# Kernel tuning notes

Hardware: AMD Instinct MI355X
Metric: run time of the kernel (lower is better)

Reference implementation:

```python
import jax, jax.numpy as jnp
import numpy as np

D_MODEL = 512
NHEAD = 8
HEAD_DIM = D_MODEL // NHEAD
DFF = 2048
RANK = 64
L = 1024
N = 8
EPS = 1e-5


def _layer_norm(x, g, b):
    m = jnp.mean(x, axis=-1, keepdims=True)
    v = jnp.mean(jnp.square(x - m), axis=-1, keepdims=True)
    return (x - m) * jax.lax.rsqrt(v + EPS) * g + b


def setup_inputs() -> dict:
    key = jax.random.key(0)
    ks = jax.random.split(key, 20)
    s = 1.0 / np.sqrt(D_MODEL)
    inp = {
        "q": jax.random.normal(ks[0], (L, N, D_MODEL), jnp.float32),
        "k": jax.random.normal(ks[1], (L, N, D_MODEL), jnp.float32),
        "v": jax.random.normal(ks[2], (L, N, D_MODEL), jnp.float32),
        # attention projections, stored (in, out) so x @ W
        "Wq": jax.random.normal(ks[3], (D_MODEL, D_MODEL), jnp.float32) * s,
        "bq": jnp.zeros((D_MODEL,), jnp.float32),
        "Wk": jax.random.normal(ks[4], (D_MODEL, D_MODEL), jnp.float32) * s,
        "bk": jnp.zeros((D_MODEL,), jnp.float32),
        "Wv": jax.random.normal(ks[5], (D_MODEL, D_MODEL), jnp.float32) * s,
        "bv": jnp.zeros((D_MODEL,), jnp.float32),
        "Wo": jax.random.normal(ks[6], (D_MODEL, D_MODEL), jnp.float32) * s,
        "bo": jnp.zeros((D_MODEL,), jnp.float32),
        "topk": jnp.float32(0.3),  # learned scalar, k = int(S * sigmoid(topk))
        "A1": jax.random.normal(ks[7], (D_MODEL, RANK), jnp.float32) * s,
        "B1": jax.random.normal(ks[8], (RANK, DFF), jnp.float32) / np.sqrt(RANK),
        "A2": jax.random.normal(ks[9], (DFF, RANK), jnp.float32) / np.sqrt(DFF),
        "B2": jax.random.normal(ks[10], (RANK, D_MODEL), jnp.float32) / np.sqrt(RANK),
        "g1": jnp.ones((D_MODEL,), jnp.float32),
        "be1": jnp.zeros((D_MODEL,), jnp.float32),
        "g2": jnp.ones((D_MODEL,), jnp.float32),
        "be2": jnp.zeros((D_MODEL,), jnp.float32),
    }
    return inp


def reference(q, k, v, Wq, bq, Wk, bk, Wv, bv, Wo, bo, topk,
              A1, B1, A2, B2, g1, be1, g2, be2):
    Lq, Nb, E = q.shape
    S = k.shape[0]
    H, Dh = NHEAD, HEAD_DIM

    # projections -> (N, L, H, Dh)
    qh = (q @ Wq + bq).reshape(Lq, Nb, H, Dh).transpose(1, 0, 2, 3)
    kh = (k @ Wk + bk).reshape(S, Nb, H, Dh).transpose(1, 0, 2, 3)
    vh = (v @ Wv + bv).reshape(S, Nb, H, Dh).transpose(1, 0, 2, 3)

    scores = jnp.einsum('nlhd,nshd->nlhs', qh, kh) / jnp.sqrt(jnp.float32(Dh))

    # dynamic top-k mask: keep the k = int(S * sigmoid(topk)) largest per row
    k_keep = (S * jax.nn.sigmoid(topk)).astype(jnp.int32)  # 588 for topk=0.3
    sorted_desc = jnp.sort(scores, axis=-1)[..., ::-1]
    idx = jnp.broadcast_to(k_keep - 1, scores.shape[:-1])[..., None]
    thresh = jnp.take_along_axis(sorted_desc, idx, axis=-1)  # k-th largest
    masked = jnp.where(scores >= thresh, scores, -jnp.inf)
    attn_w = jax.nn.softmax(masked, axis=-1)

    # note original flattens (d, h) order: 'nlhs,nshd->nldh' then view(L,N,E)
    ao = jnp.einsum('nlhs,nshd->nldh', attn_w, vh)
    ao = ao.transpose(1, 0, 2, 3).reshape(Lq, Nb, E)
    attn_out = ao @ Wo + bo

    src = _layer_norm(q + attn_out, g1, be1)
    ffn = jax.nn.relu(src @ A1 @ B1) @ A2 @ B2
    src = _layer_norm(src + ffn, g2, be2)
    return src
```

## Files before the change

### kernel.cpp

```cpp
#include <hip/hip_runtime.h>

typedef unsigned short u16;
typedef unsigned int u32;
using s16x8 = __attribute__((ext_vector_type(8))) short;
using s16x4 = __attribute__((ext_vector_type(4))) short;
using u16x4 = __attribute__((ext_vector_type(4))) unsigned short;
using u32x4 = __attribute__((ext_vector_type(4))) unsigned int;
using f32x4 = __attribute__((ext_vector_type(4))) float;

__device__ __forceinline__ u16 f2bf(float f) {
  unsigned int u = __float_as_uint(f);
  u += 0x7FFFu + ((u >> 16) & 1u);
  return (u16)(u >> 16);
}
__device__ __forceinline__ float bf2f(u16 b) {
  return __uint_as_float(((u32)b) << 16);
}
__device__ __forceinline__ u32 pkbf(float a, float b) {
  u32 r;
  asm("v_cvt_pk_bf16_f32 %0, %1, %2" : "=v"(r) : "v"(a), "v"(b));
  return r;
}
__device__ __forceinline__ u32 f2key(float f) {
  u32 u = __float_as_uint(f);
  u32 flip = (u32)((int)u >> 31) | 0x80000000u;
  return (u ^ flip) >> 16;
}
__device__ __forceinline__ float key2f(u32 k) {
  u32 t = k << 16;
  u32 msk = ((int)t < 0) ? 0x80000000u : 0xFFFF0000u;
  return __uint_as_float(t ^ msk);
}

__global__ __launch_bounds__(256) void prep_w(
    const float* __restrict__ Wq, const float* __restrict__ Wk, const float* __restrict__ Wv,
    const float* __restrict__ Wo, const float* __restrict__ A1, const float* __restrict__ B1,
    const float* __restrict__ A2, const float* __restrict__ B2,
    u16* __restrict__ WqT, u16* __restrict__ WkT, u16* __restrict__ WvT, u16* __restrict__ WoT,
    u16* __restrict__ A1T, u16* __restrict__ B1T, u16* __restrict__ A2T, u16* __restrict__ B2T) {
  __shared__ u16 t[64][68];
  int b = blockIdx.x, tid = threadIdx.x;
  const float* src; u16* dst; int base, R, C;
  if (b < 64)        { src = Wq; dst = WqT; base = 0;   R = 512;  C = 512; }
  else if (b < 128)  { src = Wk; dst = WkT; base = 64;  R = 512;  C = 512; }
  else if (b < 192)  { src = Wv; dst = WvT; base = 128; R = 512;  C = 512; }
  else if (b < 256)  { src = Wo; dst = WoT; base = 192; R = 512;  C = 512; }
  else if (b < 264)  { src = A1; dst = A1T; base = 256; R = 512;  C = 64;  }
  else if (b < 296)  { src = B1; dst = B1T; base = 264; R = 64;   C = 2048;}
  else if (b < 328)  { src = A2; dst = A2T; base = 296; R = 2048; C = 64;  }
  else               { src = B2; dst = B2T; base = 328; R = 64;   C = 512; }
  int ti = b - base;
  int tpr = C >> 6;
  int r0 = (ti / tpr) * 64, c0 = (ti % tpr) * 64;
#pragma unroll
  for (int i = 0; i < 4; ++i) {
    int r = i * 16 + (tid >> 4), c = (tid & 15) * 4;
    float4 f = *(const float4*)&src[(size_t)(r0 + r) * C + c0 + c];
    t[r][c] = f2bf(f.x); t[r][c + 1] = f2bf(f.y);
    t[r][c + 2] = f2bf(f.z); t[r][c + 3] = f2bf(f.w);
  }
  __syncthreads();
#pragma unroll
  for (int i = 0; i < 4; ++i) {
    int cc = i * 16 + (tid >> 4), rr = (tid & 15) * 4;
    u16x4 o;
    o[0] = t[rr][cc]; o[1] = t[rr + 1][cc]; o[2] = t[rr + 2][cc]; o[3] = t[rr + 3][cc];
    *(u16x4*)&dst[(size_t)(c0 + cc) * R + r0 + rr] = o;
  }
}

__global__ __launch_bounds__(256, 4) void qkv_fused(
    const float* __restrict__ q, const float* __restrict__ k, const float* __restrict__ v,
    const u16* __restrict__ WqT, const u16* __restrict__ WkT, const u16* __restrict__ WvT,
    const float* __restrict__ bq, const float* __restrict__ bk, const float* __restrict__ bv,
    u16* __restrict__ Qw, u16* __restrict__ Kw, u16* __restrict__ Vw) {
  __shared__ __align__(16) u16 As[128][72];
  __shared__ __align__(16) u16 Bs[128][72];
  const int z = blockIdx.z;
  const float* A = z == 0 ? q : (z == 1 ? k : v);
  const u16* Bt = z == 0 ? WqT : (z == 1 ? WkT : WvT);
  const float* bias = z == 0 ? bq : (z == 1 ? bk : bv);
  u16* outp = z == 0 ? Qw : (z == 1 ? Kw : Vw);

  const int tid = threadIdx.x;
  const int m0 = blockIdx.y * 128, n0 = blockIdx.x * 128;
  const int lane = tid & 63, wid = tid >> 6;
  const int l16 = lane & 15, hi = lane >> 4;
  const int wr = (wid >> 1) * 64, wc = (wid & 1) * 64;

  f32x4 acc[4][4];
#pragma unroll
  for (int i = 0; i < 4; ++i)
#pragma unroll
    for (int j = 0; j < 4; ++j) acc[i][j] = (f32x4){0.f, 0.f, 0.f, 0.f};

  for (int k0 = 0; k0 < 512; k0 += 64) {
    if (k0) __syncthreads();
#pragma unroll
    for (int i = 0; i < 4; ++i) {
      int idx = i * 256 + tid;
      int r = idx >> 3, cc = (idx & 7) * 8;
      float4 f0 = *(const float4*)&A[(size_t)(m0 + r) * 512 + k0 + cc];
      float4 f1 = *(const float4*)&A[(size_t)(m0 + r) * 512 + k0 + cc + 4];
      u32x4 pk;
      pk[0] = pkbf(f0.x, f0.y); pk[1] = pkbf(f0.z, f0.w);
      pk[2] = pkbf(f1.x, f1.y); pk[3] = pkbf(f1.z, f1.w);
      *(u32x4*)&As[r][cc] = pk;
      *(s16x8*)&Bs[r][cc] = *(const s16x8*)&Bt[(size_t)(n0 + r) * 512 + k0 + cc];
    }
    __syncthreads();
#pragma unroll
    for (int kk = 0; kk < 2; ++kk) {
      const int kb_ = kk * 32 + hi * 8;
      s16x8 af[4], bf[4];
#pragma unroll
      for (int mf = 0; mf < 4; ++mf) af[mf] = *(const s16x8*)&As[wr + mf * 16 + l16][kb_];
#pragma unroll
      for (int nf = 0; nf < 4; ++nf) bf[nf] = *(const s16x8*)&Bs[wc + nf * 16 + l16][kb_];
#pragma unroll
      for (int mf = 0; mf < 4; ++mf)
#pragma unroll
        for (int nf = 0; nf < 4; ++nf)
          acc[mf][nf] = __builtin_amdgcn_mfma_f32_16x16x32_bf16(af[mf], bf[nf], acc[mf][nf], 0, 0, 0);
    }
  }

#pragma unroll
  for (int mf = 0; mf < 4; ++mf)
#pragma unroll
    for (int nf = 0; nf < 4; ++nf)
#pragma unroll
      for (int i = 0; i < 4; ++i) {
        int row = m0 + wr + mf * 16 + hi * 4 + i;
        int col = n0 + wc + nf * 16 + l16;
        float val = acc[mf][nf][i] + bias[col];
        if (z == 0) val *= 0.18033688f;
        int l = row >> 3, n = row & 7, hh = col >> 6, d = col & 63;
        if (z < 2)
          outp[(((size_t)(n * 8 + hh) * 1024 + l) << 6) + d] = f2bf(val);
        else
          outp[((size_t)(n * 8 + hh) * 64 + d) * 1024 + l] = f2bf(val);
      }
}

__global__ __launch_bounds__(512, 4) void attn_kernel(const u16* __restrict__ Qw,
                                                      const u16* __restrict__ Kw,
                                                      const u16* __restrict__ Vw,
                                                      const float* __restrict__ topk,
                                                      u16* __restrict__ ao) {
  __shared__ __align__(16) u16 scb[32 * 1024];
  __shared__ __align__(16) u16 Qt[32][72];
  __shared__ float invs[32];
  const int tid = threadIdx.x, lane = tid & 63, wid = tid >> 6;
  const int l16 = lane & 15, hi = lane >> 4;
  const int mb = blockIdx.x, nh = blockIdx.y;

  const int kkeep = (int)(1024.f / (1.f + __expf(-topk[0])));

  {
    int r = tid >> 4, dc = (tid & 15) << 2;
    *(s16x4*)&Qt[r][dc] =
        *(const s16x4*)&Qw[((size_t)nh * 1024 + mb * 32 + r) * 64 + dc];
  }
  __syncthreads();

  {
    const u16* Kb = Kw + (size_t)nh * 1024 * 64;
    s16x8 bq0[2], bq1[2];
#pragma unroll
    for (int qh = 0; qh < 2; ++qh) {
      bq0[qh] = *(const s16x8*)&Qt[qh * 16 + l16][hi * 8];
      bq1[qh] = *(const s16x8*)&Qt[qh * 16 + l16][32 + hi * 8];
    }
    const int s0 = wid * 128;
#pragma unroll
    for (int nf = 0; nf < 8; ++nf) {
      const int sr = s0 + nf * 16 + l16;
      s16x8 a0 = *(const s16x8*)&Kb[(size_t)sr * 64 + hi * 8];
      s16x8 a1 = *(const s16x8*)&Kb[(size_t)sr * 64 + 32 + hi * 8];
#pragma unroll
      for (int qh = 0; qh < 2; ++qh) {
        f32x4 acc = {0.f, 0.f, 0.f, 0.f};
        acc = __builtin_amdgcn_mfma_f32_16x16x32_bf16(a0, bq0[qh], acc, 0, 0, 0);
        acc = __builtin_amdgcn_mfma_f32_16x16x32_bf16(a1, bq1[qh], acc, 0, 0, 0);
        const int row_q = qh * 16 + l16;
        u32 k0 = f2key(acc[0]) | (f2key(acc[1]) << 16);
        u32 k1 = f2key(acc[2]) | (f2key(acc[3]) << 16);
        char* rowq = (char*)scb + row_q * 2048;
        int boff = (2 * (s0 + nf * 16 + 4 * hi)) ^ ((row_q & 7) << 4);
        *(uint2*)(rowq + boff) = make_uint2(k0, k1);
      }
    }
  }
  __syncthreads();

  {
    const int r = wid * 4;
    char* rb0 = (char*)scb + (r + 0) * 2048;
    char* rb1 = (char*)scb + (r + 1) * 2048;
    char* rb2 = (char*)scb + (r + 2) * 2048;
    char* rb3 = (char*)scb + (r + 3) * 2048;
    const int X0 = ((r + 0) & 7) << 4, X1 = ((r + 1) & 7) << 4;
    const int X2 = ((r + 2) & 7) << 4, X3 = ((r + 3) & 7) << 4;
    u32 k0a[16], k1a[16], k2a[16], k3a[16];
#pragma unroll
    for (int c = 0; c < 8; ++c) {
      u32 w0 = *(const u32*)(rb0 + ((4 * lane + 256 * c) ^ X0));
      u32 w1 = *(const u32*)(rb1 + ((4 * lane + 256 * c) ^ X1));
      u32 w2 = *(const u32*)(rb2 + ((4 * lane + 256 * c) ^ X2));
      u32 w3 = *(const u32*)(rb3 + ((4 * lane + 256 * c) ^ X3));
      k0a[2 * c] = w0 & 0xFFFFu; k0a[2 * c + 1] = w0 >> 16;
      k1a[2 * c] = w1 & 0xFFFFu; k1a[2 * c + 1] = w1 >> 16;
      k2a[2 * c] = w2 & 0xFFFFu; k2a[2 * c + 1] = w2 >> 16;
      k3a[2 * c] = w3 & 0xFFFFu; k3a[2 * c + 1] = w3 >> 16;
    }
    u32 T0 = 0, T1 = 0, T2 = 0, T3 = 0;
    for (int bit = 15; bit >= 0; --bit) {
      const u32 bb = 1u << bit;
      u32 c0 = T0 + bb, c1 = T1 + bb, c2 = T2 + bb, c3 = T3 + bb;
      int n0 = 0, n1 = 0, n2 = 0, n3 = 0;
#pragma unroll
      for (int j = 0; j < 16; ++j) {
        n0 += __popcll(__ballot(k0a[j] >= c0));
        n1 += __popcll(__ballot(k1a[j] >= c1));
        n2 += __popcll(__ballot(k2a[j] >= c2));
        n3 += __popcll(__ballot(k3a[j] >= c3));
      }
      T0 = (n0 >= kkeep) ? c0 : T0;
      T1 = (n1 >= kkeep) ? c1 : T1;
      T2 = (n2 >= kkeep) ? c2 : T2;
      T3 = (n3 >= kkeep) ? c3 : T3;
    }
    const float tv0 = key2f(T0), tv1 = key2f(T1), tv2 = key2f(T2), tv3 = key2f(T3);
    float s0 = 0.f, s1 = 0.f, s2 = 0.f, s3 = 0.f;
#pragma unroll
    for (int c = 0; c < 8; ++c) {
      {
        u32 ka = k0a[2 * c], kb = k0a[2 * c + 1];
        float e0 = (ka >= T0) ? __builtin_amdgcn_exp2f(key2f(ka) - tv0) : 0.f;
        float e1 = (kb >= T0) ? __builtin_amdgcn_exp2f(key2f(kb) - tv0) : 0.f;
        s0 += e0 + e1;
        *(u32*)(rb0 + ((4 * lane + 256 * c) ^ X0)) = pkbf(e0, e1);
      }
      {
        u32 ka = k1a[2 * c], kb = k1a[2 * c + 1];
        float e0 = (ka >= T1) ? __builtin_amdgcn_exp2f(key2f(ka) - tv1) : 0.f;
        float e1 = (kb >= T1) ? __builtin_amdgcn_exp2f(key2f(kb) - tv1) : 0.f;
        s1 += e0 + e1;
        *(u32*)(rb1 + ((4 * lane + 256 * c) ^ X1)) = pkbf(e0, e1);
      }
      {
        u32 ka = k2a[2 * c], kb = k2a[2 * c + 1];
        float e0 = (ka >= T2) ? __builtin_amdgcn_exp2f(key2f(ka) - tv2) : 0.f;
        float e1 = (kb >= T2) ? __builtin_amdgcn_exp2f(key2f(kb) - tv2) : 0.f;
        s2 += e0 + e1;
        *(u32*)(rb2 + ((4 * lane + 256 * c) ^ X2)) = pkbf(e0, e1);
      }
      {
        u32 ka = k3a[2 * c], kb = k3a[2 * c + 1];
        float e0 = (ka >= T3) ? __builtin_amdgcn_exp2f(key2f(ka) - tv3) : 0.f;
        float e1 = (kb >= T3) ? __builtin_amdgcn_exp2f(key2f(kb) - tv3) : 0.f;
        s3 += e0 + e1;
        *(u32*)(rb3 + ((4 * lane + 256 * c) ^ X3)) = pkbf(e0, e1);
      }
    }
#pragma unroll
    for (int off = 1; off < 64; off <<= 1) {
      s0 += __shfl_xor(s0, off);
      s1 += __shfl_xor(s1, off);
      s2 += __shfl_xor(s2, off);
      s3 += __shfl_xor(s3, off);
    }
    if (lane == 0) {
      invs[r + 0] = __builtin_amdgcn_rcpf(s0);
      invs[r + 1] = __builtin_amdgcn_rcpf(s1);
      invs[r + 2] = __builtin_amdgcn_rcpf(s2);
      invs[r + 3] = __builtin_amdgcn_rcpf(s3);
    }
  }
  __syncthreads();

  {
    const u16* Vb = Vw + (size_t)nh * 64 * 1024;
    const int rh = wid >> 2, d0 = (wid & 3) * 16;
    f32x4 oacc0 = {0.f, 0.f, 0.f, 0.f};
    f32x4 oacc1 = {0.f, 0.f, 0.f, 0.f};
    const char* Pbase = (const char*)scb + (rh * 16 + l16) * 2048;
    const int Xp = (l16 & 7) << 4;
#pragma unroll
    for (int ks = 0; ks < 32; ks += 2) {
      int kb0 = (ks * 64 + hi * 16) ^ Xp;
      int kb1 = ((ks + 1) * 64 + hi * 16) ^ Xp;
      s16x8 a0 = *(const s16x8*)(Pbase + kb0);
      s16x8 a1 = *(const s16x8*)(Pbase + kb1);
      s16x8 b0 = *(const s16x8*)&Vb[(size_t)(d0 + l16) * 1024 + ks * 32 + hi * 8];
      s16x8 b1 = *(const s16x8*)&Vb[(size_t)(d0 + l16) * 1024 + (ks + 1) * 32 + hi * 8];
      oacc0 = __builtin_amdgcn_mfma_f32_16x16x32_bf16(a0, b0, oacc0, 0, 0, 0);
      oacc1 = __builtin_amdgcn_mfma_f32_16x16x32_bf16(a1, b1, oacc1, 0, 0, 0);
    }
    const int n = nh >> 3, hh = nh & 7;
#pragma unroll
    for (int i = 0; i < 4; ++i) {
      int l = mb * 32 + rh * 16 + hi * 4 + i;
      int d = d0 + l16;
      float vv = (oacc0[i] + oacc1[i]) * invs[rh * 16 + hi * 4 + i];
      ao[(size_t)(l * 8 + n) * 512 + d * 8 + hh] = f2bf(vv);
    }
  }
}

template <bool FIRST>
__global__ __launch_bounds__(256, 2) void gemm_ln(const u16* __restrict__ A,
                                                  const u16* __restrict__ Bt,
                                                  const float* __restrict__ bias,
                                                  const float* __restrict__ residf,
                                                  const u16* __restrict__ residb,
                                                  const float* __restrict__ g,
                                                  const float* __restrict__ be,
                                                  float* __restrict__ outf,
                                                  u16* __restrict__ outb) {
  constexpr int K = FIRST ? 512 : 64;
  __shared__ __align__(16) u16 As[16][72];
  __shared__ float red_s[4][16];
  __shared__ float red_q[4][16];
  const int tid = threadIdx.x;
  const int lane = tid & 63, wid = tid >> 6;
  const int l16 = lane & 15, hi = lane >> 4;
  const int m0 = blockIdx.x * 16;
  const int wc = wid * 128;

  f32x4 acc[8];
#pragma unroll
  for (int nf = 0; nf < 8; ++nf) acc[nf] = (f32x4){0.f, 0.f, 0.f, 0.f};

  for (int k0 = 0; k0 < K; k0 += 64) {
    if (k0) __syncthreads();
    {
      int r = tid >> 4, c = (tid & 15) << 2;
      *(s16x4*)&As[r][c] = *(const s16x4*)&A[(size_t)(m0 + r) * K + k0 + c];
    }
    __syncthreads();
#pragma unroll
    for (int kk = 0; kk < 2; ++kk) {
      const int kb_ = kk * 32 + hi * 8;
      s16x8 a = *(const s16x8*)&As[l16][kb_];
#pragma unroll
      for (int nf = 0; nf < 8; ++nf) {
        s16x8 b = *(const s16x8*)&Bt[(size_t)(wc + nf * 16 + l16) * K + k0 + kb_];
        acc[nf] = __builtin_amdgcn_mfma_f32_16x16x32_bf16(a, b, acc[nf], 0, 0, 0);
      }
    }
  }

#pragma unroll
  for (int nf = 0; nf < 8; ++nf) {
    int col = wc + nf * 16 + l16;
#pragma unroll
    for (int i = 0; i < 4; ++i) {
      float v = acc[nf][i];
      int row = m0 + hi * 4 + i;
      if (FIRST) v += bias[col] + residf[(size_t)row * 512 + col];
      else v += bf2f(residb[(size_t)row * 512 + col]);
      acc[nf][i] = v;
    }
  }
  float s[4] = {0.f, 0.f, 0.f, 0.f}, q2[4] = {0.f, 0.f, 0.f, 0.f};
#pragma unroll
  for (int nf = 0; nf < 8; ++nf)
#pragma unroll
    for (int i = 0; i < 4; ++i) {
      s[i] += acc[nf][i];
      q2[i] += acc[nf][i] * acc[nf][i];
    }
#pragma unroll
  for (int i = 0; i < 4; ++i) {
#pragma unroll
    for (int off = 1; off < 16; off <<= 1) {
      s[i] += __shfl_xor(s[i], off);
      q2[i] += __shfl_xor(q2[i], off);
    }
  }
  if (l16 == 0) {
#pragma unroll
    for (int i = 0; i < 4; ++i) {
      red_s[wid][hi * 4 + i] = s[i];
      red_q[wid][hi * 4 + i] = q2[i];
    }
  }
  __syncthreads();
  float mean[4], rstd[4];
#pragma unroll
  for (int i = 0; i < 4; ++i) {
    int r = hi * 4 + i;
    float ms = red_s[0][r] + red_s[1][r] + red_s[2][r] + red_s[3][r];
    float mq = red_q[0][r] + red_q[1][r] + red_q[2][r] + red_q[3][r];
    mean[i] = ms * (1.f / 512.f);
    float var = mq * (1.f / 512.f) - mean[i] * mean[i];
    rstd[i] = rsqrtf(var + 1e-5f);
  }
#pragma unroll
  for (int nf = 0; nf < 8; ++nf) {
    int col = wc + nf * 16 + l16;
    float gv = g[col], bev = be[col];
#pragma unroll
    for (int i = 0; i < 4; ++i) {
      int row = m0 + hi * 4 + i;
      float y = (acc[nf][i] - mean[i]) * rstd[i] * gv + bev;
      if (FIRST) outb[(size_t)row * 512 + col] = f2bf(y);
      else outf[(size_t)row * 512 + col] = y;
    }
  }
}

__global__ __launch_bounds__(256, 4) void ffn3(const u16* __restrict__ srcb,
                                               const u16* __restrict__ A1T,
                                               const u16* __restrict__ B1T,
                                               const u16* __restrict__ A2T,
                                               u16* __restrict__ w2) {
  __shared__ __align__(16) u16 As[32][72];
  __shared__ __align__(16) u16 Bs[64][72];
  __shared__ __align__(16) u16 Us[32][72];
  __shared__ __align__(16) u16 B1s[64][72];
  __shared__ __align__(16) u16 A2s[64][72];
  __shared__ __align__(16) u16 Hs[32][72];
  const int tid = threadIdx.x;
  const int lane = tid & 63, wid = tid >> 6;
  const int l16 = lane & 15, hi = lane >> 4;
  const int m0 = blockIdx.x * 32;
  const int wm = (wid & 1) * 16, wn = (wid >> 1) * 32;

  f32x4 accu[2];
  accu[0] = (f32x4){0.f, 0.f, 0.f, 0.f};
  accu[1] = (f32x4){0.f, 0.f, 0.f, 0.f};
  for (int k0 = 0; k0 < 512; k0 += 64) {
    if (k0) __syncthreads();
    {
      int r = tid >> 3, c = (tid & 7) << 3;
      *(s16x8*)&As[r][c] = *(const s16x8*)&srcb[(size_t)(m0 + r) * 512 + k0 + c];
    }
#pragma unroll
    for (int i = 0; i < 2; ++i) {
      int idx = i * 256 + tid;
      int r = idx >> 3, c = (idx & 7) << 3;
      *(s16x8*)&Bs[r][c] = *(const s16x8*)&A1T[(size_t)r * 512 + k0 + c];
    }
    __syncthreads();
#pragma unroll
    for (int kk = 0; kk < 2; ++kk) {
      const int kb_ = kk * 32 + hi * 8;
      s16x8 a = *(const s16x8*)&As[wm + l16][kb_];
#pragma unroll
      for (int j = 0; j < 2; ++j) {
        s16x8 b = *(const s16x8*)&Bs[wn + j * 16 + l16][kb_];
        accu[j] = __builtin_amdgcn_mfma_f32_16x16x32_bf16(a, b, accu[j], 0, 0, 0);
      }
    }
  }
  __syncthreads();
#pragma unroll
  for (int j = 0; j < 2; ++j)
#pragma unroll
    for (int i = 0; i < 4; ++i)
      Us[wm + hi * 4 + i][wn + j * 16 + l16] = f2bf(accu[j][i]);

  f32x4 w2a[2];
  w2a[0] = (f32x4){0.f, 0.f, 0.f, 0.f};
  w2a[1] = (f32x4){0.f, 0.f, 0.f, 0.f};
  for (int jc = 0; jc < 32; ++jc) {
#pragma unroll
    for (int i = 0; i < 2; ++i) {
      int idx = i * 256 + tid;
      int r = idx >> 3, c = (idx & 7) << 3;
      *(s16x8*)&B1s[r][c] = *(const s16x8*)&B1T[(size_t)(jc * 64 + r) * 64 + c];
      *(s16x8*)&A2s[r][c] = *(const s16x8*)&A2T[(size_t)r * 2048 + jc * 64 + c];
    }
    __syncthreads();
    f32x4 ha[2];
    ha[0] = (f32x4){0.f, 0.f, 0.f, 0.f};
    ha[1] = (f32x4){0.f, 0.f, 0.f, 0.f};
#pragma unroll
    for (int kk = 0; kk < 2; ++kk) {
      const int kb_ = kk * 32 + hi * 8;
      s16x8 a = *(const s16x8*)&Us[wm + l16][kb_];
#pragma unroll
      for (int j = 0; j < 2; ++j) {
        s16x8 b = *(const s16x8*)&B1s[wn + j * 16 + l16][kb_];
        ha[j] = __builtin_amdgcn_mfma_f32_16x16x32_bf16(a, b, ha[j], 0, 0, 0);
      }
    }
#pragma unroll
    for (int j = 0; j < 2; ++j)
#pragma unroll
      for (int i = 0; i < 4; ++i)
        Hs[wm + hi * 4 + i][wn + j * 16 + l16] = f2bf(fmaxf(ha[j][i], 0.f));
    __syncthreads();
#pragma unroll
    for (int kk = 0; kk < 2; ++kk) {
      const int kb_ = kk * 32 + hi * 8;
      s16x8 a = *(const s16x8*)&Hs[wm + l16][kb_];
#pragma unroll
      for (int j = 0; j < 2; ++j) {
        s16x8 b = *(const s16x8*)&A2s[wn + j * 16 + l16][kb_];
        w2a[j] = __builtin_amdgcn_mfma_f32_16x16x32_bf16(a, b, w2a[j], 0, 0, 0);
      }
    }
    __syncthreads();
  }
#pragma unroll
  for (int j = 0; j < 2; ++j)
#pragma unroll
    for (int i = 0; i < 4; ++i)
      w2[(size_t)(m0 + wm + hi * 4 + i) * 64 + wn + j * 16 + l16] = f2bf(w2a[j][i]);
}

extern "C" void kernel_launch(void* const* d_in, const int* in_sizes, int n_in,
                              void* d_out, int out_size, void* d_ws, size_t ws_size,
                              hipStream_t stream) {
  const float* q = (const float*)d_in[0];
  const float* k = (const float*)d_in[1];
  const float* v = (const float*)d_in[2];
  const float* Wq = (const float*)d_in[3];
  const float* bq = (const float*)d_in[4];
  const float* Wk = (const float*)d_in[5];
  const float* bk = (const float*)d_in[6];
  const float* Wv = (const float*)d_in[7];
  const float* bv = (const float*)d_in[8];
  const float* Wo = (const float*)d_in[9];
  const float* bo = (const float*)d_in[10];
  const float* topk = (const float*)d_in[11];
  const float* A1 = (const float*)d_in[12];
  const float* B1 = (const float*)d_in[13];
  const float* A2 = (const float*)d_in[14];
  const float* B2 = (const float*)d_in[15];
  const float* g1 = (const float*)d_in[16];
  const float* be1 = (const float*)d_in[17];
  const float* g2 = (const float*)d_in[18];
  const float* be2 = (const float*)d_in[19];

  char* ws = (char*)d_ws;
  constexpr size_t SZ_TOK_BF = (size_t)8192 * 512 * 2;
  constexpr size_t SZ_W_BF = (size_t)512 * 512 * 2;
  constexpr size_t O_QW = 0;
  constexpr size_t O_KW = O_QW + SZ_TOK_BF;
  constexpr size_t O_VW = O_KW + SZ_TOK_BF;
  constexpr size_t O_WQT = O_VW + SZ_TOK_BF;
  constexpr size_t O_WKT = O_WQT + SZ_W_BF;
  constexpr size_t O_WVT = O_WKT + SZ_W_BF;
  constexpr size_t O_WOT = O_WVT + SZ_W_BF;
  constexpr size_t O_A1T = O_WOT + SZ_W_BF;
  constexpr size_t O_B1T = O_A1T + 65536;
  constexpr size_t O_A2T = O_B1T + 262144;
  constexpr size_t O_B2T = O_A2T + 262144;
  constexpr size_t O_AO = O_B2T + 65536;
  constexpr size_t O_SRCB = O_AO + SZ_TOK_BF;
  constexpr size_t O_W2 = O_SRCB + SZ_TOK_BF;

  u16* Qw_ = (u16*)(ws + O_QW);
  u16* Kw_ = (u16*)(ws + O_KW);
  u16* Vw_ = (u16*)(ws + O_VW);
  u16* WqT = (u16*)(ws + O_WQT);
  u16* WkT = (u16*)(ws + O_WKT);
  u16* WvT = (u16*)(ws + O_WVT);
  u16* WoT = (u16*)(ws + O_WOT);
  u16* A1T = (u16*)(ws + O_A1T);
  u16* B1T = (u16*)(ws + O_B1T);
  u16* A2T = (u16*)(ws + O_A2T);
  u16* B2T = (u16*)(ws + O_B2T);
  u16* ao = (u16*)(ws + O_AO);
  u16* srcb = (u16*)(ws + O_SRCB);
  u16* w2 = (u16*)(ws + O_W2);

  prep_w<<<336, 256, 0, stream>>>(Wq, Wk, Wv, Wo, A1, B1, A2, B2,
                                  WqT, WkT, WvT, WoT, A1T, B1T, A2T, B2T);

  qkv_fused<<<dim3(4, 64, 3), 256, 0, stream>>>(q, k, v, WqT, WkT, WvT,
                                                bq, bk, bv, Qw_, Kw_, Vw_);

  attn_kernel<<<dim3(32, 64), 512, 0, stream>>>(Qw_, Kw_, Vw_, topk, ao);

  gemm_ln<true><<<512, 256, 0, stream>>>(ao, WoT, bo, q, nullptr, g1, be1, nullptr, srcb);

  ffn3<<<256, 256, 0, stream>>>(srcb, A1T, B1T, A2T, w2);

  gemm_ln<false><<<512, 256, 0, stream>>>(w2, B2T, nullptr, nullptr, srcb, g2, be2,
                                          (float*)d_out, nullptr);
}
```

Before: 286.6 us.

## Pre-convert q/k/v to bf16, prefetch K/V fragments, vectorize score LDS traffic

```diff
diff --git a/kernel.cpp b/kernel.cpp
--- a/kernel.cpp
+++ b/kernel.cpp
@@ -32,14 +32,27 @@
   return __uint_as_float(t ^ msk);
 }
 
-__global__ __launch_bounds__(256) void prep_w(
+__global__ __launch_bounds__(256) void prep_all(
+    const float* __restrict__ q, const float* __restrict__ k, const float* __restrict__ v,
     const float* __restrict__ Wq, const float* __restrict__ Wk, const float* __restrict__ Wv,
     const float* __restrict__ Wo, const float* __restrict__ A1, const float* __restrict__ B1,
     const float* __restrict__ A2, const float* __restrict__ B2,
+    u16* __restrict__ qb, u16* __restrict__ kb, u16* __restrict__ vb,
     u16* __restrict__ WqT, u16* __restrict__ WkT, u16* __restrict__ WvT, u16* __restrict__ WoT,
     u16* __restrict__ A1T, u16* __restrict__ B1T, u16* __restrict__ A2T, u16* __restrict__ B2T) {
   __shared__ u16 t[64][68];
   int b = blockIdx.x, tid = threadIdx.x;
+  if (b < 12288) {
+    const float* src = b < 4096 ? q : (b < 8192 ? k : v);
+    u16* dst = b < 4096 ? qb : (b < 8192 ? kb : vb);
+    int i = (b & 4095) * 256 + tid;
+    float4 f = ((const float4*)src)[i];
+    u16x4 o;
+    o[0] = f2bf(f.x); o[1] = f2bf(f.y); o[2] = f2bf(f.z); o[3] = f2bf(f.w);
+    ((u16x4*)dst)[i] = o;
+    return;
+  }
+  b -= 12288;
   const float* src; u16* dst; int base, R, C;
   if (b < 64)        { src = Wq; dst = WqT; base = 0;   R = 512;  C = 512; }
   else if (b < 128)  { src = Wk; dst = WkT; base = 64;  R = 512;  C = 512; }
@@ -70,14 +83,14 @@
 }
 
 __global__ __launch_bounds__(256, 4) void qkv_fused(
-    const float* __restrict__ q, const float* __restrict__ k, const float* __restrict__ v,
+    const u16* __restrict__ qb, const u16* __restrict__ kb, const u16* __restrict__ vb,
     const u16* __restrict__ WqT, const u16* __restrict__ WkT, const u16* __restrict__ WvT,
     const float* __restrict__ bq, const float* __restrict__ bk, const float* __restrict__ bv,
     u16* __restrict__ Qw, u16* __restrict__ Kw, u16* __restrict__ Vw) {
   __shared__ __align__(16) u16 As[128][72];
   __shared__ __align__(16) u16 Bs[128][72];
   const int z = blockIdx.z;
-  const float* A = z == 0 ? q : (z == 1 ? k : v);
+  const u16* A = z == 0 ? qb : (z == 1 ? kb : vb);
   const u16* Bt = z == 0 ? WqT : (z == 1 ? WkT : WvT);
   const float* bias = z == 0 ? bq : (z == 1 ? bk : bv);
   u16* outp = z == 0 ? Qw : (z == 1 ? Kw : Vw);
@@ -100,12 +113,7 @@
     for (int i = 0; i < 4; ++i) {
       int idx = i * 256 + tid;
       int r = idx >> 3, cc = (idx & 7) * 8;
-      float4 f0 = *(const float4*)&A[(size_t)(m0 + r) * 512 + k0 + cc];
-      float4 f1 = *(const float4*)&A[(size_t)(m0 + r) * 512 + k0 + cc + 4];
-      u32x4 pk;
-      pk[0] = pkbf(f0.x, f0.y); pk[1] = pkbf(f0.z, f0.w);
-      pk[2] = pkbf(f1.x, f1.y); pk[3] = pkbf(f1.z, f1.w);
-      *(u32x4*)&As[r][cc] = pk;
+      *(s16x8*)&As[r][cc] = *(const s16x8*)&A[(size_t)(m0 + r) * 512 + k0 + cc];
       *(s16x8*)&Bs[r][cc] = *(const s16x8*)&Bt[(size_t)(n0 + r) * 512 + k0 + cc];
     }
     __syncthreads();
@@ -173,16 +181,22 @@
       bq1[qh] = *(const s16x8*)&Qt[qh * 16 + l16][32 + hi * 8];
     }
     const int s0 = wid * 128;
+    const size_t kbase = (size_t)(s0 + l16) * 64 + hi * 8;
+    s16x8 c0 = *(const s16x8*)&Kb[kbase];
+    s16x8 c1 = *(const s16x8*)&Kb[kbase + 32];
 #pragma unroll
     for (int nf = 0; nf < 8; ++nf) {
-      const int sr = s0 + nf * 16 + l16;
-      s16x8 a0 = *(const s16x8*)&Kb[(size_t)sr * 64 + hi * 8];
-      s16x8 a1 = *(const s16x8*)&Kb[(size_t)sr * 64 + 32 + hi * 8];
+      s16x8 n0_, n1_;
+      if (nf < 7) {
+        const size_t nb = kbase + (size_t)(nf + 1) * 1024;
+        n0_ = *(const s16x8*)&Kb[nb];
+        n1_ = *(const s16x8*)&Kb[nb + 32];
+      }
 #pragma unroll
       for (int qh = 0; qh < 2; ++qh) {
         f32x4 acc = {0.f, 0.f, 0.f, 0.f};
-        acc = __builtin_amdgcn_mfma_f32_16x16x32_bf16(a0, bq0[qh], acc, 0, 0, 0);
-        acc = __builtin_amdgcn_mfma_f32_16x16x32_bf16(a1, bq1[qh], acc, 0, 0, 0);
+        acc = __builtin_amdgcn_mfma_f32_16x16x32_bf16(c0, bq0[qh], acc, 0, 0, 0);
+        acc = __builtin_amdgcn_mfma_f32_16x16x32_bf16(c1, bq1[qh], acc, 0, 0, 0);
         const int row_q = qh * 16 + l16;
         u32 k0 = f2key(acc[0]) | (f2key(acc[1]) << 16);
         u32 k1 = f2key(acc[2]) | (f2key(acc[3]) << 16);
@@ -190,6 +204,7 @@
         int boff = (2 * (s0 + nf * 16 + 4 * hi)) ^ ((row_q & 7) << 4);
         *(uint2*)(rowq + boff) = make_uint2(k0, k1);
       }
+      c0 = n0_; c1 = n1_;
     }
   }
   __syncthreads();
@@ -202,17 +217,25 @@
     char* rb3 = (char*)scb + (r + 3) * 2048;
     const int X0 = ((r + 0) & 7) << 4, X1 = ((r + 1) & 7) << 4;
     const int X2 = ((r + 2) & 7) << 4, X3 = ((r + 3) & 7) << 4;
+    const int o0 = (16 * lane) ^ X0, o0b = (16 * lane + 1024) ^ X0;
+    const int o1 = (16 * lane) ^ X1, o1b = (16 * lane + 1024) ^ X1;
+    const int o2 = (16 * lane) ^ X2, o2b = (16 * lane + 1024) ^ X2;
+    const int o3 = (16 * lane) ^ X3, o3b = (16 * lane + 1024) ^ X3;
+    u32x4 q0a = *(const u32x4*)(rb0 + o0), q0b = *(const u32x4*)(rb0 + o0b);
+    u32x4 q1a = *(const u32x4*)(rb1 + o1), q1b = *(const u32x4*)(rb1 + o1b);
+    u32x4 q2a = *(const u32x4*)(rb2 + o2), q2b = *(const u32x4*)(rb2 + o2b);
+    u32x4 q3a = *(const u32x4*)(rb3 + o3), q3b = *(const u32x4*)(rb3 + o3b);
     u32 k0a[16], k1a[16], k2a[16], k3a[16];
 #pragma unroll
-    for (int c = 0; c < 8; ++c) {
-      u32 w0 = *(const u32*)(rb0 + ((4 * lane + 256 * c) ^ X0));
-      u32 w1 = *(const u32*)(rb1 + ((4 * lane + 256 * c) ^ X1));
-      u32 w2 = *(const u32*)(rb2 + ((4 * lane + 256 * c) ^ X2));
-      u32 w3 = *(const u32*)(rb3 + ((4 * lane + 256 * c) ^ X3));
-      k0a[2 * c] = w0 & 0xFFFFu; k0a[2 * c + 1] = w0 >> 16;
-      k1a[2 * c] = w1 & 0xFFFFu; k1a[2 * c + 1] = w1 >> 16;
-      k2a[2 * c] = w2 & 0xFFFFu; k2a[2 * c + 1] = w2 >> 16;
-      k3a[2 * c] = w3 & 0xFFFFu; k3a[2 * c + 1] = w3 >> 16;
+    for (int j = 0; j < 4; ++j) {
+      k0a[2 * j] = q0a[j] & 0xFFFFu; k0a[2 * j + 1] = q0a[j] >> 16;
+      k0a[8 + 2 * j] = q0b[j] & 0xFFFFu; k0a[9 + 2 * j] = q0b[j] >> 16;
+      k1a[2 * j] = q1a[j] & 0xFFFFu; k1a[2 * j + 1] = q1a[j] >> 16;
+      k1a[8 + 2 * j] = q1b[j] & 0xFFFFu; k1a[9 + 2 * j] = q1b[j] >> 16;
+      k2a[2 * j] = q2a[j] & 0xFFFFu; k2a[2 * j + 1] = q2a[j] >> 16;
+      k2a[8 + 2 * j] = q2b[j] & 0xFFFFu; k2a[9 + 2 * j] = q2b[j] >> 16;
+      k3a[2 * j] = q3a[j] & 0xFFFFu; k3a[2 * j + 1] = q3a[j] >> 16;
+      k3a[8 + 2 * j] = q3b[j] & 0xFFFFu; k3a[9 + 2 * j] = q3b[j] >> 16;
     }
     u32 T0 = 0, T1 = 0, T2 = 0, T3 = 0;
     for (int bit = 15; bit >= 0; --bit) {
@@ -233,37 +256,46 @@
     }
     const float tv0 = key2f(T0), tv1 = key2f(T1), tv2 = key2f(T2), tv3 = key2f(T3);
     float s0 = 0.f, s1 = 0.f, s2 = 0.f, s3 = 0.f;
-#pragma unroll
-    for (int c = 0; c < 8; ++c) {
+    u32x4 w0a, w0b, w1a, w1b, w2a_, w2b, w3a, w3b;
+#pragma unroll
+    for (int j = 0; j < 4; ++j) {
       {
-        u32 ka = k0a[2 * c], kb = k0a[2 * c + 1];
-        float e0 = (ka >= T0) ? __builtin_amdgcn_exp2f(key2f(ka) - tv0) : 0.f;
-        float e1 = (kb >= T0) ? __builtin_amdgcn_exp2f(key2f(kb) - tv0) : 0.f;
-        s0 += e0 + e1;
-        *(u32*)(rb0 + ((4 * lane + 256 * c) ^ X0)) = pkbf(e0, e1);
+        float e0 = (k0a[2 * j] >= T0) ? __builtin_amdgcn_exp2f(key2f(k0a[2 * j]) - tv0) : 0.f;
+        float e1 = (k0a[2 * j + 1] >= T0) ? __builtin_amdgcn_exp2f(key2f(k0a[2 * j + 1]) - tv0) : 0.f;
+        float e2 = (k0a[8 + 2 * j] >= T0) ? __builtin_amdgcn_exp2f(key2f(k0a[8 + 2 * j]) - tv0) : 0.f;
+        float e3 = (k0a[9 + 2 * j] >= T0) ? __builtin_amdgcn_exp2f(key2f(k0a[9 + 2 * j]) - tv0) : 0.f;
+        s0 += e0 + e1 + e2 + e3;
+        w0a[j] = pkbf(e0, e1); w0b[j] = pkbf(e2, e3);
       }
       {
-        u32 ka = k1a[2 * c], kb = k1a[2 * c + 1];
-        float e0 = (ka >= T1) ? __builtin_amdgcn_exp2f(key2f(ka) - tv1) : 0.f;
-        float e1 = (kb >= T1) ? __builtin_amdgcn_exp2f(key2f(kb) - tv1) : 0.f;
-        s1 += e0 + e1;
-        *(u32*)(rb1 + ((4 * lane + 256 * c) ^ X1)) = pkbf(e0, e1);
+        float e0 = (k1a[2 * j] >= T1) ? __builtin_amdgcn_exp2f(key2f(k1a[2 * j]) - tv1) : 0.f;
+        float e1 = (k1a[2 * j + 1] >= T1) ? __builtin_amdgcn_exp2f(key2f(k1a[2 * j + 1]) - tv1) : 0.f;
+        float e2 = (k1a[8 + 2 * j] >= T1) ? __builtin_amdgcn_exp2f(key2f(k1a[8 + 2 * j]) - tv1) : 0.f;
+        float e3 = (k1a[9 + 2 * j] >= T1) ? __builtin_amdgcn_exp2f(key2f(k1a[9 + 2 * j]) - tv1) : 0.f;
+        s1 += e0 + e1 + e2 + e3;
+        w1a[j] = pkbf(e0, e1); w1b[j] = pkbf(e2, e3);
       }
       {
-        u32 ka = k2a[2 * c], kb = k2a[2 * c + 1];
-        float e0 = (ka >= T2) ? __builtin_amdgcn_exp2f(key2f(ka) - tv2) : 0.f;
-        float e1 = (kb >= T2) ? __builtin_amdgcn_exp2f(key2f(kb) - tv2) : 0.f;
-        s2 += e0 + e1;
-        *(u32*)(rb2 + ((4 * lane + 256 * c) ^ X2)) = pkbf(e0, e1);
+        float e0 = (k2a[2 * j] >= T2) ? __builtin_amdgcn_exp2f(key2f(k2a[2 * j]) - tv2) : 0.f;
+        float e1 = (k2a[2 * j + 1] >= T2) ? __builtin_amdgcn_exp2f(key2f(k2a[2 * j + 1]) - tv2) : 0.f;
+        float e2 = (k2a[8 + 2 * j] >= T2) ? __builtin_amdgcn_exp2f(key2f(k2a[8 + 2 * j]) - tv2) : 0.f;
+        float e3 = (k2a[9 + 2 * j] >= T2) ? __builtin_amdgcn_exp2f(key2f(k2a[9 + 2 * j]) - tv2) : 0.f;
+        s2 += e0 + e1 + e2 + e3;
+        w2a_[j] = pkbf(e0, e1); w2b[j] = pkbf(e2, e3);
       }
       {
-        u32 ka = k3a[2 * c], kb = k3a[2 * c + 1];
-        float e0 = (ka >= T3) ? __builtin_amdgcn_exp2f(key2f(ka) - tv3) : 0.f;
-        float e1 = (kb >= T3) ? __builtin_amdgcn_exp2f(key2f(kb) - tv3) : 0.f;
-        s3 += e0 + e1;
-        *(u32*)(rb3 + ((4 * lane + 256 * c) ^ X3)) = pkbf(e0, e1);
-      }
-    }
+        float e0 = (k3a[2 * j] >= T3) ? __builtin_amdgcn_exp2f(key2f(k3a[2 * j]) - tv3) : 0.f;
+        float e1 = (k3a[2 * j + 1] >= T3) ? __builtin_amdgcn_exp2f(key2f(k3a[2 * j + 1]) - tv3) : 0.f;
+        float e2 = (k3a[8 + 2 * j] >= T3) ? __builtin_amdgcn_exp2f(key2f(k3a[8 + 2 * j]) - tv3) : 0.f;
+        float e3 = (k3a[9 + 2 * j] >= T3) ? __builtin_amdgcn_exp2f(key2f(k3a[9 + 2 * j]) - tv3) : 0.f;
+        s3 += e0 + e1 + e2 + e3;
+        w3a[j] = pkbf(e0, e1); w3b[j] = pkbf(e2, e3);
+      }
+    }
+    *(u32x4*)(rb0 + o0) = w0a; *(u32x4*)(rb0 + o0b) = w0b;
+    *(u32x4*)(rb1 + o1) = w1a; *(u32x4*)(rb1 + o1b) = w1b;
+    *(u32x4*)(rb2 + o2) = w2a_; *(u32x4*)(rb2 + o2b) = w2b;
+    *(u32x4*)(rb3 + o3) = w3a; *(u32x4*)(rb3 + o3b) = w3b;
 #pragma unroll
     for (int off = 1; off < 64; off <<= 1) {
       s0 += __shfl_xor(s0, off);
@@ -287,16 +319,21 @@
     f32x4 oacc1 = {0.f, 0.f, 0.f, 0.f};
     const char* Pbase = (const char*)scb + (rh * 16 + l16) * 2048;
     const int Xp = (l16 & 7) << 4;
+    const size_t vbase = (size_t)(d0 + l16) * 1024 + hi * 8;
+    s16x8 v0 = *(const s16x8*)&Vb[vbase];
+    s16x8 v1 = *(const s16x8*)&Vb[vbase + 32];
 #pragma unroll
     for (int ks = 0; ks < 32; ks += 2) {
-      int kb0 = (ks * 64 + hi * 16) ^ Xp;
-      int kb1 = ((ks + 1) * 64 + hi * 16) ^ Xp;
-      s16x8 a0 = *(const s16x8*)(Pbase + kb0);
-      s16x8 a1 = *(const s16x8*)(Pbase + kb1);
-      s16x8 b0 = *(const s16x8*)&Vb[(size_t)(d0 + l16) * 1024 + ks * 32 + hi * 8];
-      s16x8 b1 = *(const s16x8*)&Vb[(size_t)(d0 + l16) * 1024 + (ks + 1) * 32 + hi * 8];
-      oacc0 = __builtin_amdgcn_mfma_f32_16x16x32_bf16(a0, b0, oacc0, 0, 0, 0);
-      oacc1 = __builtin_amdgcn_mfma_f32_16x16x32_bf16(a1, b1, oacc1, 0, 0, 0);
+      s16x8 nv0, nv1;
+      if (ks < 30) {
+        nv0 = *(const s16x8*)&Vb[vbase + (size_t)(ks + 2) * 32];
+        nv1 = *(const s16x8*)&Vb[vbase + (size_t)(ks + 3) * 32];
+      }
+      s16x8 a0 = *(const s16x8*)(Pbase + ((ks * 64 + hi * 16) ^ Xp));
+      s16x8 a1 = *(const s16x8*)(Pbase + (((ks + 1) * 64 + hi * 16) ^ Xp));
+      oacc0 = __builtin_amdgcn_mfma_f32_16x16x32_bf16(a0, v0, oacc0, 0, 0, 0);
+      oacc1 = __builtin_amdgcn_mfma_f32_16x16x32_bf16(a1, v1, oacc1, 0, 0, 0);
+      v0 = nv0; v1 = nv1;
     }
     const int n = nh >> 3, hh = nh & 7;
 #pragma unroll
@@ -540,7 +577,10 @@
   char* ws = (char*)d_ws;
   constexpr size_t SZ_TOK_BF = (size_t)8192 * 512 * 2;
   constexpr size_t SZ_W_BF = (size_t)512 * 512 * 2;
-  constexpr size_t O_QW = 0;
+  constexpr size_t O_QB = 0;
+  constexpr size_t O_KB = O_QB + SZ_TOK_BF;
+  constexpr size_t O_VB = O_KB + SZ_TOK_BF;
+  constexpr size_t O_QW = O_VB + SZ_TOK_BF;
   constexpr size_t O_KW = O_QW + SZ_TOK_BF;
   constexpr size_t O_VW = O_KW + SZ_TOK_BF;
   constexpr size_t O_WQT = O_VW + SZ_TOK_BF;
@@ -555,6 +595,9 @@
   constexpr size_t O_SRCB = O_AO + SZ_TOK_BF;
   constexpr size_t O_W2 = O_SRCB + SZ_TOK_BF;
 
+  u16* qb = (u16*)(ws + O_QB);
+  u16* kb = (u16*)(ws + O_KB);
+  u16* vb = (u16*)(ws + O_VB);
   u16* Qw_ = (u16*)(ws + O_QW);
   u16* Kw_ = (u16*)(ws + O_KW);
   u16* Vw_ = (u16*)(ws + O_VW);
@@ -570,10 +613,10 @@
   u16* srcb = (u16*)(ws + O_SRCB);
   u16* w2 = (u16*)(ws + O_W2);
 
-  prep_w<<<336, 256, 0, stream>>>(Wq, Wk, Wv, Wo, A1, B1, A2, B2,
-                                  WqT, WkT, WvT, WoT, A1T, B1T, A2T, B2T);
-
-  qkv_fused<<<dim3(4, 64, 3), 256, 0, stream>>>(q, k, v, WqT, WkT, WvT,
+  prep_all<<<12624, 256, 0, stream>>>(q, k, v, Wq, Wk, Wv, Wo, A1, B1, A2, B2,
+                                      qb, kb, vb, WqT, WkT, WvT, WoT, A1T, B1T, A2T, B2T);
+
+  qkv_fused<<<dim3(4, 64, 3), 256, 0, stream>>>(qb, kb, vb, WqT, WkT, WvT,
                                                 bq, bk, bv, Qw_, Kw_, Vw_);
 
   attn_kernel<<<dim3(32, 64), 512, 0, stream>>>(Qw_, Kw_, Vw_, topk, ao);
```

Measured after the change: 291.3 us. Within noise of the previous version (+1.6%).
